# Performance work log

Measured on AMD Instinct MI355X. Metric: run time of the kernel, lower is better.

Reference implementation:

```python
import jax, jax.numpy as jnp
import numpy as np

NPG = 128      # nodes per graph = g(4) * e(32), forced by rearrange + cnn1 channels
G, E32 = 4, 32
ALPHA = 1.0    # GCN2Conv(in_channels, 1) -> alpha = 1
BETA = 1.0     # theta=None -> beta = 1


def _gcn_norm(edge_index, edge_weight, n):
    """PyG gcn_norm: add self-loops (w=1), sym-normalize by degree at dst."""
    src, dst = edge_index[0], edge_index[1]
    loop = jnp.arange(n)
    src = jnp.concatenate([src, loop])
    dst = jnp.concatenate([dst, loop])
    w = jnp.concatenate([edge_weight, jnp.ones((n,), edge_weight.dtype)])
    deg = jax.ops.segment_sum(w, dst, num_segments=n)
    dinv = jnp.where(deg > 0, jax.lax.rsqrt(deg), 0.0)
    norm = dinv[src] * w * dinv[dst]
    return src, dst, norm


def _propagate(x, src, dst, norm, n):
    # gather -> weight -> scatter-add (SpMM)
    return jax.ops.segment_sum(x[src] * norm[:, None], dst, num_segments=n)


def setup_inputs() -> dict:
    key = jax.random.key(0)
    ks = jax.random.split(key, 10)
    N, E, C, H, CH = 65536, 524288, 128, 512, 256
    x = jax.random.normal(ks[0], (N, C), jnp.float32)
    edge_index = jax.random.randint(ks[1], (2, E), 0, N, dtype=jnp.int64)
    edge_attr = jax.random.uniform(ks[2], (E,), jnp.float32)
    w1_gcn2 = jax.random.normal(ks[3], (C, C), jnp.float32) / np.float32(np.sqrt(C))
    w_gcn = jax.random.normal(ks[4], (C, H), jnp.float32) / np.float32(np.sqrt(C))
    b_gcn = jnp.zeros((H,), jnp.float32)
    w_cnn1 = jax.random.normal(ks[5], (H, 4 * H), jnp.float32) / np.float32(np.sqrt(4 * H))
    b_cnn1 = jnp.zeros((H,), jnp.float32)
    w_cnn2 = jax.random.normal(ks[6], (CH, H), jnp.float32) / np.float32(np.sqrt(H))
    b_cnn2 = jnp.zeros((CH,), jnp.float32)
    w_lin = jax.random.normal(ks[7], (32 * CH,), jnp.float32) / np.float32(np.sqrt(32 * CH))
    b_lin = jnp.zeros((), jnp.float32)
    return {"x": x, "edge_attr": edge_attr, "w1_gcn2": w1_gcn2, "w_gcn": w_gcn,
            "b_gcn": b_gcn, "w_cnn1": w_cnn1, "b_cnn1": b_cnn1, "w_cnn2": w_cnn2,
            "b_cnn2": b_cnn2, "w_lin": w_lin, "b_lin": b_lin, "edge_index": edge_index}


def reference(x, edge_attr, w1_gcn2, w_gcn, b_gcn, w_cnn1, b_cnn1, w_cnn2, b_cnn2,
              w_lin, b_lin, edge_index):
    n = x.shape[0]
    bs = n // NPG
    src, dst, norm = _gcn_norm(edge_index, edge_attr, n)

    # GCN2Conv(C, layer=1): h = (1-a)*A_hat x + a*x0; out = (1-b)*h + b*(h @ W1)
    h = _propagate(x, src, dst, norm, n)
    h = h * (1.0 - ALPHA) + ALPHA * x
    h = (1.0 - BETA) * h + BETA * (h @ w1_gcn2)

    # GCNConv(C, H): A_hat (h @ W) + b
    h = _propagate(h @ w_gcn, src, dst, norm, n) + b_gcn
    h = jnp.tanh(h)

    f = h.shape[1]  # hidden_channels
    # '(bs g e) f -> bs (g f) e', e=32, g=4
    h = h.reshape(bs, G, E32, f).transpose(0, 1, 3, 2).reshape(bs, G * f, E32)
    # 1x1 convs == per-position linears over channel dim
    h = jax.nn.relu(jnp.einsum('bce,oc->boe', h, w_cnn1) + b_cnn1[None, :, None])
    h = jax.nn.relu(jnp.einsum('bce,oc->boe', h, w_cnn2) + b_cnn2[None, :, None])
    # dropout p=0.5 is identity in eval mode
    h = h.reshape(bs, -1)
    out = h @ w_lin + b_lin
    return jax.nn.sigmoid(out)
```

## Files before the change

### kernel.cpp

```cpp
#include <hip/hip_runtime.h>
#include <hip/hip_bf16.h>

#define N_NODES 65536
#define N_EDGES 524288

typedef __attribute__((ext_vector_type(8))) short bf16x8;
typedef __attribute__((ext_vector_type(4))) float f32x4;

__device__ __forceinline__ float bf2f(unsigned short u) {
    union { unsigned int i; float f; } v;
    v.i = ((unsigned int)u) << 16;
    return v.f;
}
__device__ __forceinline__ unsigned short f2bf(float f) {
    union { float f; unsigned int i; } v;
    v.f = f;
    unsigned int r = v.i + 0x7fff + ((v.i >> 16) & 1);
    return (unsigned short)(r >> 16);
}

__global__ void init_k(int* __restrict__ cnt, float* __restrict__ logits) {
    int i = blockIdx.x * 256 + threadIdx.x;
    cnt[i] = 0;
    if (i < 512) logits[i] = 0.0f;
}
__global__ void cnt_k(const int* __restrict__ dst, int* __restrict__ cnt) {
    int e = blockIdx.x * 256 + threadIdx.x;
    atomicAdd(&cnt[dst[e]], 1);
}

__global__ __launch_bounds__(256) void scan1_k(const int* __restrict__ cnt,
                                               int* __restrict__ rp,
                                               int* __restrict__ bsum) {
    __shared__ int s[256];
    int t = threadIdx.x, g = blockIdx.x * 256 + t;
    int v = cnt[g];
    s[t] = v;
    __syncthreads();
    for (int d = 1; d < 256; d <<= 1) {
        int u = (t >= d) ? s[t - d] : 0;
        __syncthreads();
        s[t] += u;
        __syncthreads();
    }
    rp[g] = s[t] - v;
    if (t == 255) bsum[blockIdx.x] = s[255];
}
__global__ __launch_bounds__(256) void scan2_k(int* __restrict__ bsum,
                                               int* __restrict__ rp) {
    __shared__ int s[256];
    int t = threadIdx.x;
    int v = bsum[t];
    s[t] = v;
    __syncthreads();
    for (int d = 1; d < 256; d <<= 1) {
        int u = (t >= d) ? s[t - d] : 0;
        __syncthreads();
        s[t] += u;
        __syncthreads();
    }
    bsum[t] = s[t] - v;
    if (t == 255) rp[65536] = s[255];
}
__global__ __launch_bounds__(256) void scan3_k(int* __restrict__ rp,
                                               const int* __restrict__ bsum,
                                               int* __restrict__ cursor) {
    int t = threadIdx.x, g = blockIdx.x * 256 + t;
    int r = rp[g] + bsum[blockIdx.x];
    rp[g] = r;
    cursor[g] = r;
}

__global__ void scatter_k(const int* __restrict__ src, const int* __restrict__ dst,
                          const float* __restrict__ w,
                          int* __restrict__ cursor, uint2* __restrict__ ep) {
    int e = blockIdx.x * 256 + threadIdx.x;
    int pos = atomicAdd(&cursor[dst[e]], 1);
    uint2 p;
    p.x = (unsigned int)src[e];
    p.y = __float_as_uint(w[e]);
    ep[pos] = p;
}

__global__ void rowsum_k(const int* __restrict__ rp, const uint2* __restrict__ ep,
                         float* __restrict__ dinv) {
    int n = blockIdx.x * 256 + threadIdx.x;
    int beg = rp[n], end = rp[n + 1];
    float s = 1.0f;
    for (int i = beg; i < end; ++i) s += __uint_as_float(ep[i].y);
    dinv[n] = rsqrtf(s);
}

__global__ void xscale_k(const float* __restrict__ x, const float* __restrict__ dinv,
                         __hip_bfloat16* __restrict__ xbf) {
    int i = (blockIdx.x * 256 + threadIdx.x) * 4;
    float d = dinv[i >> 7];
    float4 v = *(const float4*)(x + i);
    alignas(8) __hip_bfloat16 tmp[4] = {
        __float2bfloat16(d * v.x), __float2bfloat16(d * v.y),
        __float2bfloat16(d * v.z), __float2bfloat16(d * v.w)};
    *(ushort4*)((unsigned short*)xbf + i) = *(const ushort4*)tmp;
}

__global__ void wprep_k(const float* __restrict__ wc1, __hip_bfloat16* __restrict__ wc1pk,
                        const float* __restrict__ wc2, __hip_bfloat16* __restrict__ wc2bf,
                        const float* __restrict__ w1, const float* __restrict__ wg,
                        __hip_bfloat16* __restrict__ WTpk) {
    int bid = blockIdx.x;
    if (bid < 512) {
        int t = bid * 256 + threadIdx.x;
        int l = t & 63, grp = t >> 6;
        int kt = grp & 63, nb = grp >> 6;
        int n = nb * 16 + (l & 15);
        int k0 = kt * 32 + (l >> 4) * 8;
        const float* src = wc1 + (size_t)n * 2048 + k0;
        alignas(16) __hip_bfloat16 tmp[8];
#pragma unroll
        for (int e = 0; e < 8; ++e) tmp[e] = __float2bfloat16(src[e]);
        *(ushort4*)((unsigned short*)wc1pk + (size_t)t * 8)     = *(const ushort4*)tmp;
        *(ushort4*)((unsigned short*)wc1pk + (size_t)t * 8 + 4) = *(const ushort4*)(tmp + 4);
    } else if (bid < 640) {
        int i = (bid - 512) * 1024 + threadIdx.x * 4;
        float4 v = *(const float4*)(wc2 + i);
        alignas(8) __hip_bfloat16 tmp[4] = {__float2bfloat16(v.x), __float2bfloat16(v.y),
                                            __float2bfloat16(v.z), __float2bfloat16(v.w)};
        *(ushort4*)((unsigned short*)wc2bf + i) = *(const ushort4*)tmp;
    } else {
        int t = (bid - 640) * 256 + threadIdx.x;
        int f = t >> 7, c = t & 127;
        float s = 0.f;
#pragma unroll 8
        for (int m = 0; m < 128; ++m) s += w1[c * 128 + m] * wg[m * 512 + f];
        int pk = ((((f >> 4) * 4 + (c >> 5)) * 64 + ((c >> 3) & 3) * 16 + (f & 15)) * 8) + (c & 7);
        WTpk[pk] = __float2bfloat16(s);
    }
}

__global__ __launch_bounds__(256) void gather_k(const int* __restrict__ rp,
                                                const uint2* __restrict__ ep,
                                                const unsigned short* __restrict__ xbf,
                                                const float* __restrict__ dinv,
                                                __hip_bfloat16* __restrict__ ybf) {
    int n = (blockIdx.x * 256 + threadIdx.x) >> 6;
    int lane = threadIdx.x & 63;
    int beg = rp[n], end = rp[n + 1];
    float accx, accy;
    {
        unsigned int u = *(const unsigned int*)(xbf + (size_t)n * 128 + lane * 2);
        accx = bf2f((unsigned short)(u & 0xffff));
        accy = bf2f((unsigned short)(u >> 16));
    }
    int i = beg;
    for (; i + 8 <= end; i += 8) {
        uint2 p[8];
        unsigned int u[8];
#pragma unroll
        for (int k = 0; k < 8; ++k) p[k] = ep[i + k];
#pragma unroll
        for (int k = 0; k < 8; ++k)
            u[k] = *(const unsigned int*)(xbf + (size_t)p[k].x * 128 + lane * 2);
#pragma unroll
        for (int k = 0; k < 8; ++k) {
            float c = __uint_as_float(p[k].y);
            accx += c * bf2f((unsigned short)(u[k] & 0xffff));
            accy += c * bf2f((unsigned short)(u[k] >> 16));
        }
    }
    for (; i + 4 <= end; i += 4) {
        uint2 p[4];
        unsigned int u[4];
#pragma unroll
        for (int k = 0; k < 4; ++k) p[k] = ep[i + k];
#pragma unroll
        for (int k = 0; k < 4; ++k)
            u[k] = *(const unsigned int*)(xbf + (size_t)p[k].x * 128 + lane * 2);
#pragma unroll
        for (int k = 0; k < 4; ++k) {
            float c = __uint_as_float(p[k].y);
            accx += c * bf2f((unsigned short)(u[k] & 0xffff));
            accy += c * bf2f((unsigned short)(u[k] >> 16));
        }
    }
    for (; i < end; ++i) {
        uint2 p = ep[i];
        unsigned int u = *(const unsigned int*)(xbf + (size_t)p.x * 128 + lane * 2);
        float c = __uint_as_float(p.y);
        accx += c * bf2f((unsigned short)(u & 0xffff));
        accy += c * bf2f((unsigned short)(u >> 16));
    }
    float dn = dinv[n];
    accx *= dn;
    accy *= dn;
    alignas(4) __hip_bfloat16 o[2] = {__float2bfloat16(accx), __float2bfloat16(accy)};
    *(unsigned int*)((unsigned short*)ybf + (size_t)n * 128 + lane * 2) =
        *(const unsigned int*)o;
}

__device__ __forceinline__ void gll16(const void* g, void* l) {
    __builtin_amdgcn_global_load_lds(
        (const __attribute__((address_space(1))) void*)g,
        (__attribute__((address_space(3))) void*)l, 16, 0, 0);
}

__global__ __launch_bounds__(512) void fh2c1_k(
    const __hip_bfloat16* __restrict__ ybf,
    const __hip_bfloat16* __restrict__ WTpk,
    const float* __restrict__ bg,
    const __hip_bfloat16* __restrict__ wc1pk,
    const float* __restrict__ bc1,
    __hip_bfloat16* __restrict__ act1) {
    __shared__ char yt[16384];
    __shared__ char ht[16384];
    const int tid = threadIdx.x;
    const int lane = tid & 63, wid = tid >> 6;
    const int bx = blockIdx.x;
    const int l15 = lane & 15, lhi = lane >> 4;

    const __hip_bfloat16* Bp[4];
#pragma unroll
    for (int j = 0; j < 4; ++j)
        Bp[j] = wc1pk + ((size_t)(wid * 4 + j) * 64) * 512 + lane * 8;

    auto stageY = [&](int buf, int g) {
        int r = wid * 4 + (lane >> 4);
        int node = bx * 128 + g * 32 + r;
        int scol = ((lane & 15) ^ (r & 7)) << 4;
        gll16((const char*)ybf + (size_t)node * 256 + scol,
              yt + buf * 8192 + wid * 1024 + lane * 16);
    };

    f32x4 acc[2][4] = {};

    stageY(0, 0);
    __syncthreads();

    for (int g = 0; g < 4; ++g) {
        if (g > 0) __syncthreads();
        const char* ytc = yt + (g & 1) * 8192;

        for (int h = 0; h < 2; ++h) {
            f32x4 hacc[2][2];
#pragma unroll
            for (int i = 0; i < 2; ++i)
#pragma unroll
                for (int j = 0; j < 2; ++j) hacc[i][j] = (f32x4){0.f, 0.f, 0.f, 0.f};
#pragma unroll
            for (int kt = 0; kt < 4; ++kt) {
                bf16x8 af[2], bfr[2];
#pragma unroll
                for (int i = 0; i < 2; ++i) {
                    int r = i * 16 + l15;
                    int s = (kt * 4 + lhi) ^ (r & 7);
                    af[i] = *(const bf16x8*)(ytc + r * 256 + s * 16);
                }
#pragma unroll
                for (int j = 0; j < 2; ++j) {
                    int nb = h * 16 + wid * 2 + j;
                    bfr[j] = *(const bf16x8*)(WTpk +
                        ((size_t)(nb * 4 + kt) * 64 + lane) * 8);
                }
#pragma unroll
                for (int i = 0; i < 2; ++i)
#pragma unroll
                    for (int j = 0; j < 2; ++j)
                        hacc[i][j] = __builtin_amdgcn_mfma_f32_16x16x32_bf16(
                            bfr[j], af[i], hacc[i][j], 0, 0, 0);
            }
            __syncthreads();
#pragma unroll
            for (int j = 0; j < 2; ++j) {
                int coln = h * 256 + wid * 32 + j * 16 + lhi * 4;
                float4 bgv = *(const float4*)(bg + coln);
                int bytecol = (wid * 32 + j * 16 + lhi * 4) * 2;
                int s = bytecol >> 4;
                int off8 = bytecol & 15;
#pragma unroll
                for (int i = 0; i < 2; ++i) {
                    int row = i * 16 + l15;
                    alignas(8) unsigned short o[4];
#pragma unroll
                    for (int r = 0; r < 4; ++r) {
                        float v = hacc[i][j][r] + ((const float*)&bgv)[r];
                        v = 1.0f - 2.0f / (__expf(2.0f * v) + 1.0f);
                        o[r] = f2bf(v);
                    }
                    *(uint2*)(ht + row * 512 + ((s ^ (row & 7)) << 4) + off8) =
                        *(const uint2*)o;
                }
            }
            __syncthreads();

            if (h == 1 && g < 3) stageY((g + 1) & 1, g + 1);

            const int ktb = g * 16 + h * 8;
            bf16x8 bb[4][4];
#pragma unroll
            for (int d = 0; d < 4; ++d)
#pragma unroll
                for (int j = 0; j < 4; ++j)
                    bb[d][j] = *(const bf16x8*)(Bp[j] + (size_t)(ktb + d) * 512);
#pragma unroll
            for (int kk = 0; kk < 8; ++kk) {
                bf16x8 af[2];
#pragma unroll
                for (int i = 0; i < 2; ++i) {
                    int r = i * 16 + l15;
                    int s = (kk * 4 + lhi) ^ (r & 7);
                    af[i] = *(const bf16x8*)(ht + r * 512 + s * 16);
                }
#pragma unroll
                for (int i = 0; i < 2; ++i)
#pragma unroll
                    for (int j = 0; j < 4; ++j)
                        acc[i][j] = __builtin_amdgcn_mfma_f32_16x16x32_bf16(
                            bb[kk & 3][j], af[i], acc[i][j], 0, 0, 0);
                if (kk + 4 < 8) {
#pragma unroll
                    for (int j = 0; j < 4; ++j)
                        bb[kk & 3][j] =
                            *(const bf16x8*)(Bp[j] + (size_t)(ktb + kk + 4) * 512);
                }
            }
        }
    }

#pragma unroll
    for (int i = 0; i < 2; ++i) {
        int m = bx * 32 + i * 16 + l15;
#pragma unroll
        for (int j = 0; j < 4; ++j) {
            int n = wid * 64 + j * 16 + lhi * 4;
            float4 bv = *(const float4*)(bc1 + n);
            ushort4 o;
#pragma unroll
            for (int r = 0; r < 4; ++r) {
                float v = fmaxf(acc[i][j][r] + ((const float*)&bv)[r], 0.f);
                ((unsigned short*)&o)[r] = f2bf(v);
            }
            *(ushort4*)((unsigned short*)act1 + (size_t)m * 512 + n) = o;
        }
    }
}

template <int ACT, int OUT_MODE, int SWIZ_NTX>
__global__ __launch_bounds__(256) void gemm_mfma_k(
    const __hip_bfloat16* __restrict__ A, const __hip_bfloat16* __restrict__ B,
    const float* __restrict__ bias, void* __restrict__ Cout,
    const float* __restrict__ wlin, int M, int N, int K) {
    __shared__ char lds[65536];

    const int tid = threadIdx.x;
    const int lane = tid & 63, wid = tid >> 6;
    int bx, by;
    if (SWIZ_NTX > 0) {
        int orig = blockIdx.x;
        int per = gridDim.x / (8 * SWIZ_NTX);
        int xcd = orig & 7, k = orig >> 3;
        by = xcd * per + k / SWIZ_NTX;
        bx = k % SWIZ_NTX;
    } else {
        bx = blockIdx.x;
        by = blockIdx.y;
    }
    const int bm = by * 128, bn = bx * 128;
    const int wr = wid >> 1, wc = wid & 1;

    const int srow = wid * 16 + (lane >> 2);
    const int skcol = (((lane & 3) ^ ((lane >> 3) & 3))) * 8;
    const __hip_bfloat16* Abase = A + (size_t)(bm + srow) * K + skcol;
    const __hip_bfloat16* Bbase = B + (size_t)(bn + srow) * K + skcol;
    const int ldso = wid * 1024;

    f32x4 acc[4][4] = {};

    const int lrow = lane & 15;
    const int lkb = (((lane >> 4) ^ ((lane >> 1) & 3)) << 4);
    const int nk = K >> 5;

    auto stage = [&](int buf, int kt) {
        char* la = lds + buf * 16384;
        char* lb = la + 8192;
        gll16(Abase + kt * 32,                  la + ldso);
        gll16(Abase + kt * 32 + (size_t)64 * K, la + 4096 + ldso);
        gll16(Bbase + kt * 32,                  lb + ldso);
        gll16(Bbase + kt * 32 + (size_t)64 * K, lb + 4096 + ldso);
    };

    stage(0, 0);
    stage(1, 1);
    stage(2, 2);

    for (int kt = 0; kt < nk; ++kt) {
        int ahead = nk - 1 - kt;
        if (ahead >= 2)      asm volatile("s_waitcnt vmcnt(8)" ::: "memory");
        else if (ahead == 1) asm volatile("s_waitcnt vmcnt(4)" ::: "memory");
        else                 asm volatile("s_waitcnt vmcnt(0)" ::: "memory");
        __builtin_amdgcn_s_barrier();
        asm volatile("" ::: "memory");
        if (kt + 3 < nk) stage((kt + 3) & 3, kt + 3);

        const char* la = lds + (kt & 3) * 16384;
        const char* lb = la + 8192;
        bf16x8 af[4], bfr[4];
#pragma unroll
        for (int i = 0; i < 4; ++i)
            af[i] = *(const bf16x8*)(la + (wr * 64 + i * 16 + lrow) * 64 + lkb);
#pragma unroll
        for (int j = 0; j < 4; ++j)
            bfr[j] = *(const bf16x8*)(lb + (wc * 64 + j * 16 + lrow) * 64 + lkb);
        __builtin_amdgcn_s_setprio(1);
#pragma unroll
        for (int i = 0; i < 4; ++i)
#pragma unroll
            for (int j = 0; j < 4; ++j)
                acc[i][j] = __builtin_amdgcn_mfma_f32_16x16x32_bf16(
                    bfr[j], af[i], acc[i][j], 0, 0, 0);
        __builtin_amdgcn_s_setprio(0);
        asm volatile("" ::: "memory");
    }

    const int l15 = lane & 15, lhi = lane >> 4;

    if (OUT_MODE == 3) {
        float p0 = 0.f, p1 = 0.f;
#pragma unroll
        for (int i = 0; i < 4; ++i) {
            int e = (i & 1) * 16 + l15;
#pragma unroll
            for (int j = 0; j < 4; ++j) {
                int n = bn + wc * 64 + j * 16 + lhi * 4;
                float4 bv = *(const float4*)(bias + n);
#pragma unroll
                for (int r = 0; r < 4; ++r) {
                    float v = fmaxf(acc[i][j][r] + ((const float*)&bv)[r], 0.f);
                    float wl = wlin[(n + r) * 32 + e];
                    if (i < 2) p0 += v * wl; else p1 += v * wl;
                }
            }
        }
#pragma unroll
        for (int off = 32; off > 0; off >>= 1) {
            p0 += __shfl_down(p0, off, 64);
            p1 += __shfl_down(p1, off, 64);
        }
        if (lane == 0) {
            int g = (bm >> 5) + wr * 2;
            atomicAdd(&((float*)Cout)[g], p0);
            atomicAdd(&((float*)Cout)[g + 1], p1);
        }
        return;
    }

#pragma unroll
    for (int i = 0; i < 4; ++i) {
        int m = bm + wr * 64 + i * 16 + l15;
#pragma unroll
        for (int j = 0; j < 4; ++j) {
            int n = bn + wc * 64 + j * 16 + lhi * 4;
            float4 bv = *(const float4*)(bias + n);
            ushort4 o;
#pragma unroll
            for (int r = 0; r < 4; ++r) {
                float v = acc[i][j][r] + ((const float*)&bv)[r];
                if (ACT == 1) v = fmaxf(v, 0.f);
                ((unsigned short*)&o)[r] = f2bf(v);
            }
            *(ushort4*)((unsigned short*)Cout + (size_t)m * N + n) = o;
        }
    }
}

__global__ void sigmoid_k(const float* __restrict__ logits,
                          const float* __restrict__ blin, float* __restrict__ out) {
    int b = blockIdx.x * 256 + threadIdx.x;
    out[b] = 1.0f / (1.0f + expf(-(logits[b] + blin[0])));
}

extern "C" void kernel_launch(void* const* d_in, const int* in_sizes, int n_in,
                              void* d_out, int out_size, void* d_ws, size_t ws_size,
                              hipStream_t stream) {
    const float* x    = (const float*)d_in[0];
    const float* eattr= (const float*)d_in[1];
    const float* w1   = (const float*)d_in[2];
    const float* wg   = (const float*)d_in[3];
    const float* bg   = (const float*)d_in[4];
    const float* wc1  = (const float*)d_in[5];
    const float* bc1  = (const float*)d_in[6];
    const float* wc2  = (const float*)d_in[7];
    const float* bc2  = (const float*)d_in[8];
    const float* wlin = (const float*)d_in[9];
    const float* blin = (const float*)d_in[10];
    const int*   ei   = (const int*)d_in[11];
    const int* esrc = ei;
    const int* edst = ei + N_EDGES;
    float* out = (float*)d_out;

    char* ws = (char*)d_ws;
    float*          dinv   = (float*)(ws + 0);
    int*            cnt    = (int*)(ws + 262144);
    int*            rp     = (int*)(ws + 524288);
    int*            cursor = (int*)(ws + 786688);
    uint2*          ep     = (uint2*)(ws + 1048832);
    __hip_bfloat16* WTpk   = (__hip_bfloat16*)(ws + 5243136);
    __hip_bfloat16* ybf    = (__hip_bfloat16*)(ws + 5374208);
    __hip_bfloat16* act1   = (__hip_bfloat16*)(ws + 89260288);
    __hip_bfloat16* wc1pk  = (__hip_bfloat16*)(ws + 106037504);
    __hip_bfloat16* wc2bf  = (__hip_bfloat16*)(ws + 108134656);
    __hip_bfloat16* xbf    = (__hip_bfloat16*)(ws + 108396800);
    float*          logits = (float*)(ws + 125174016);
    int*            bsum   = (int*)(ws + 125176064);
    if (ws_size < (size_t)125177088) return;

    init_k<<<N_NODES / 256, 256, 0, stream>>>(cnt, logits);

    cnt_k<<<N_EDGES / 256, 256, 0, stream>>>(edst, cnt);

    scan1_k<<<256, 256, 0, stream>>>(cnt, rp, bsum);
    scan2_k<<<1, 256, 0, stream>>>(bsum, rp);
    scan3_k<<<256, 256, 0, stream>>>(rp, bsum, cursor);

    scatter_k<<<N_EDGES / 256, 256, 0, stream>>>(esrc, edst, eattr, cursor, ep);

    rowsum_k<<<N_NODES / 256, 256, 0, stream>>>(rp, ep, dinv);

    wprep_k<<<896, 256, 0, stream>>>(wc1, wc1pk, wc2, wc2bf, w1, wg, WTpk);
    xscale_k<<<(N_NODES * 128 / 4) / 256, 256, 0, stream>>>(x, dinv, xbf);

    gather_k<<<N_NODES / 4, 256, 0, stream>>>(rp, ep,
                                              (const unsigned short*)xbf, dinv, ybf);

    fh2c1_k<<<512, 512, 0, stream>>>(ybf, WTpk, bg, wc1pk, bc1, act1);

    gemm_mfma_k<1, 3, 0><<<dim3(2, 128), 256, 0, stream>>>(
        act1, wc2bf, bc2, logits, wlin, 16384, 256, 512);

    sigmoid_k<<<2, 256, 0, stream>>>(logits, blin, out);
}
```

Baseline: 195.1 us.

## Fuse cnn2 GEMM, linear head and sigmoid into the cnn1 kernel

The act1 intermediate is no longer written to global memory. The cnn1 output tile is staged into swizzled LDS, and each block then runs the cnn2 GEMM with MFMA against the packed wc2 weights. It applies bias and ReLU, dot-products with w_lin, reduces across waves and writes the sigmoid output for its graph directly. This removes two kernel launches, the act1 round trip and the atomics on logits, at the cost of a longer per-block tail and cnn2 B fragments loaded straight from global memory without LDS staging.

Result: faster. 186.4 us, median of 2 (-4.5%).

```diff
diff --git a/kernel.cpp b/kernel.cpp
--- a/kernel.cpp
+++ b/kernel.cpp
@@ -19,10 +19,8 @@
     return (unsigned short)(r >> 16);
 }
 
-__global__ void init_k(int* __restrict__ cnt, float* __restrict__ logits) {
-    int i = blockIdx.x * 256 + threadIdx.x;
-    cnt[i] = 0;
-    if (i < 512) logits[i] = 0.0f;
+__global__ void init_k(int* __restrict__ cnt) {
+    cnt[blockIdx.x * 256 + threadIdx.x] = 0;
 }
 __global__ void cnt_k(const int* __restrict__ dst, int* __restrict__ cnt) {
     int e = blockIdx.x * 256 + threadIdx.x;
@@ -103,30 +101,28 @@
 }
 
 __global__ void wprep_k(const float* __restrict__ wc1, __hip_bfloat16* __restrict__ wc1pk,
-                        const float* __restrict__ wc2, __hip_bfloat16* __restrict__ wc2bf,
+                        const float* __restrict__ wc2, __hip_bfloat16* __restrict__ wc2pk,
                         const float* __restrict__ w1, const float* __restrict__ wg,
                         __hip_bfloat16* __restrict__ WTpk) {
     int bid = blockIdx.x;
-    if (bid < 512) {
-        int t = bid * 256 + threadIdx.x;
+    if (bid < 576) {
+        const float* W;
+        __hip_bfloat16* outp;
+        int t, K, nkt;
+        if (bid < 512) { W = wc1; outp = wc1pk; t = bid * 256 + threadIdx.x; K = 2048; nkt = 64; }
+        else           { W = wc2; outp = wc2pk; t = (bid - 512) * 256 + threadIdx.x; K = 512; nkt = 16; }
         int l = t & 63, grp = t >> 6;
-        int kt = grp & 63, nb = grp >> 6;
+        int kt = grp % nkt, nb = grp / nkt;
         int n = nb * 16 + (l & 15);
         int k0 = kt * 32 + (l >> 4) * 8;
-        const float* src = wc1 + (size_t)n * 2048 + k0;
+        const float* src = W + (size_t)n * K + k0;
         alignas(16) __hip_bfloat16 tmp[8];
 #pragma unroll
         for (int e = 0; e < 8; ++e) tmp[e] = __float2bfloat16(src[e]);
-        *(ushort4*)((unsigned short*)wc1pk + (size_t)t * 8)     = *(const ushort4*)tmp;
-        *(ushort4*)((unsigned short*)wc1pk + (size_t)t * 8 + 4) = *(const ushort4*)(tmp + 4);
-    } else if (bid < 640) {
-        int i = (bid - 512) * 1024 + threadIdx.x * 4;
-        float4 v = *(const float4*)(wc2 + i);
-        alignas(8) __hip_bfloat16 tmp[4] = {__float2bfloat16(v.x), __float2bfloat16(v.y),
-                                            __float2bfloat16(v.z), __float2bfloat16(v.w)};
-        *(ushort4*)((unsigned short*)wc2bf + i) = *(const ushort4*)tmp;
+        *(ushort4*)((unsigned short*)outp + (size_t)t * 8)     = *(const ushort4*)tmp;
+        *(ushort4*)((unsigned short*)outp + (size_t)t * 8 + 4) = *(const ushort4*)(tmp + 4);
     } else {
-        int t = (bid - 640) * 256 + threadIdx.x;
+        int t = (bid - 576) * 256 + threadIdx.x;
         int f = t >> 7, c = t & 127;
         float s = 0.f;
 #pragma unroll 8
@@ -208,9 +204,15 @@
     const float* __restrict__ bg,
     const __hip_bfloat16* __restrict__ wc1pk,
     const float* __restrict__ bc1,
-    __hip_bfloat16* __restrict__ act1) {
-    __shared__ char yt[16384];
-    __shared__ char ht[16384];
+    const __hip_bfloat16* __restrict__ wc2pk,
+    const float* __restrict__ bc2,
+    const float* __restrict__ wlin,
+    const float* __restrict__ blin,
+    float* __restrict__ out) {
+    __shared__ char lds[32768];
+    __shared__ float red[8];
+    char* yt = lds;
+    char* ht = lds + 16384;
     const int tid = threadIdx.x;
     const int lane = tid & 63, wid = tid >> 6;
     const int bx = blockIdx.x;
@@ -324,156 +326,85 @@
         }
     }
 
-#pragma unroll
-    for (int i = 0; i < 2; ++i) {
-        int m = bx * 32 + i * 16 + l15;
-#pragma unroll
-        for (int j = 0; j < 4; ++j) {
-            int n = wid * 64 + j * 16 + lhi * 4;
-            float4 bv = *(const float4*)(bc1 + n);
-            ushort4 o;
+    __syncthreads();
+    char* at = lds;
+
+#pragma unroll
+    for (int j = 0; j < 4; ++j) {
+        int coln = wid * 64 + j * 16 + lhi * 4;
+        float4 bv = *(const float4*)(bc1 + coln);
+        int bytecol = coln * 2;
+        int s = bytecol >> 4;
+        int off8 = bytecol & 15;
+#pragma unroll
+        for (int i = 0; i < 2; ++i) {
+            int row = i * 16 + l15;
+            alignas(8) unsigned short o[4];
 #pragma unroll
             for (int r = 0; r < 4; ++r) {
                 float v = fmaxf(acc[i][j][r] + ((const float*)&bv)[r], 0.f);
-                ((unsigned short*)&o)[r] = f2bf(v);
+                o[r] = f2bf(v);
             }
-            *(ushort4*)((unsigned short*)act1 + (size_t)m * 512 + n) = o;
-        }
-    }
-}
-
-template <int ACT, int OUT_MODE, int SWIZ_NTX>
-__global__ __launch_bounds__(256) void gemm_mfma_k(
-    const __hip_bfloat16* __restrict__ A, const __hip_bfloat16* __restrict__ B,
-    const float* __restrict__ bias, void* __restrict__ Cout,
-    const float* __restrict__ wlin, int M, int N, int K) {
-    __shared__ char lds[65536];
-
-    const int tid = threadIdx.x;
-    const int lane = tid & 63, wid = tid >> 6;
-    int bx, by;
-    if (SWIZ_NTX > 0) {
-        int orig = blockIdx.x;
-        int per = gridDim.x / (8 * SWIZ_NTX);
-        int xcd = orig & 7, k = orig >> 3;
-        by = xcd * per + k / SWIZ_NTX;
-        bx = k % SWIZ_NTX;
-    } else {
-        bx = blockIdx.x;
-        by = blockIdx.y;
-    }
-    const int bm = by * 128, bn = bx * 128;
-    const int wr = wid >> 1, wc = wid & 1;
-
-    const int srow = wid * 16 + (lane >> 2);
-    const int skcol = (((lane & 3) ^ ((lane >> 3) & 3))) * 8;
-    const __hip_bfloat16* Abase = A + (size_t)(bm + srow) * K + skcol;
-    const __hip_bfloat16* Bbase = B + (size_t)(bn + srow) * K + skcol;
-    const int ldso = wid * 1024;
-
-    f32x4 acc[4][4] = {};
-
-    const int lrow = lane & 15;
-    const int lkb = (((lane >> 4) ^ ((lane >> 1) & 3)) << 4);
-    const int nk = K >> 5;
-
-    auto stage = [&](int buf, int kt) {
-        char* la = lds + buf * 16384;
-        char* lb = la + 8192;
-        gll16(Abase + kt * 32,                  la + ldso);
-        gll16(Abase + kt * 32 + (size_t)64 * K, la + 4096 + ldso);
-        gll16(Bbase + kt * 32,                  lb + ldso);
-        gll16(Bbase + kt * 32 + (size_t)64 * K, lb + 4096 + ldso);
-    };
-
-    stage(0, 0);
-    stage(1, 1);
-    stage(2, 2);
-
-    for (int kt = 0; kt < nk; ++kt) {
-        int ahead = nk - 1 - kt;
-        if (ahead >= 2)      asm volatile("s_waitcnt vmcnt(8)" ::: "memory");
-        else if (ahead == 1) asm volatile("s_waitcnt vmcnt(4)" ::: "memory");
-        else                 asm volatile("s_waitcnt vmcnt(0)" ::: "memory");
-        __builtin_amdgcn_s_barrier();
-        asm volatile("" ::: "memory");
-        if (kt + 3 < nk) stage((kt + 3) & 3, kt + 3);
-
-        const char* la = lds + (kt & 3) * 16384;
-        const char* lb = la + 8192;
-        bf16x8 af[4], bfr[4];
-#pragma unroll
-        for (int i = 0; i < 4; ++i)
-            af[i] = *(const bf16x8*)(la + (wr * 64 + i * 16 + lrow) * 64 + lkb);
-#pragma unroll
-        for (int j = 0; j < 4; ++j)
-            bfr[j] = *(const bf16x8*)(lb + (wc * 64 + j * 16 + lrow) * 64 + lkb);
-        __builtin_amdgcn_s_setprio(1);
-#pragma unroll
-        for (int i = 0; i < 4; ++i)
-#pragma unroll
-            for (int j = 0; j < 4; ++j)
-                acc[i][j] = __builtin_amdgcn_mfma_f32_16x16x32_bf16(
-                    bfr[j], af[i], acc[i][j], 0, 0, 0);
-        __builtin_amdgcn_s_setprio(0);
-        asm volatile("" ::: "memory");
-    }
-
-    const int l15 = lane & 15, lhi = lane >> 4;
-
-    if (OUT_MODE == 3) {
-        float p0 = 0.f, p1 = 0.f;
-#pragma unroll
-        for (int i = 0; i < 4; ++i) {
-            int e = (i & 1) * 16 + l15;
-#pragma unroll
-            for (int j = 0; j < 4; ++j) {
-                int n = bn + wc * 64 + j * 16 + lhi * 4;
-                float4 bv = *(const float4*)(bias + n);
-#pragma unroll
-                for (int r = 0; r < 4; ++r) {
-                    float v = fmaxf(acc[i][j][r] + ((const float*)&bv)[r], 0.f);
-                    float wl = wlin[(n + r) * 32 + e];
-                    if (i < 2) p0 += v * wl; else p1 += v * wl;
-                }
+            *(uint2*)(at + row * 1024 + ((s ^ (row & 7)) << 4) + off8) =
+                *(const uint2*)o;
+        }
+    }
+    __syncthreads();
+
+    const __hip_bfloat16* Cp[2];
+#pragma unroll
+    for (int j = 0; j < 2; ++j)
+        Cp[j] = wc2pk + ((size_t)(wid * 2 + j) * 16) * 512 + lane * 8;
+    f32x4 cacc[2][2];
+#pragma unroll
+    for (int i = 0; i < 2; ++i)
+#pragma unroll
+        for (int j = 0; j < 2; ++j) cacc[i][j] = (f32x4){0.f, 0.f, 0.f, 0.f};
+#pragma unroll
+    for (int kt = 0; kt < 16; ++kt) {
+        bf16x8 af[2], bfr[2];
+#pragma unroll
+        for (int i = 0; i < 2; ++i) {
+            int r = i * 16 + l15;
+            int s = (kt * 4 + lhi) ^ (r & 7);
+            af[i] = *(const bf16x8*)(at + r * 1024 + s * 16);
+        }
+#pragma unroll
+        for (int j = 0; j < 2; ++j)
+            bfr[j] = *(const bf16x8*)(Cp[j] + (size_t)kt * 512);
+#pragma unroll
+        for (int i = 0; i < 2; ++i)
+#pragma unroll
+            for (int j = 0; j < 2; ++j)
+                cacc[i][j] = __builtin_amdgcn_mfma_f32_16x16x32_bf16(
+                    bfr[j], af[i], cacc[i][j], 0, 0, 0);
+    }
+
+    float part = 0.f;
+#pragma unroll
+    for (int i = 0; i < 2; ++i) {
+        int e = i * 16 + l15;
+#pragma unroll
+        for (int j = 0; j < 2; ++j) {
+            int p = wid * 32 + j * 16 + lhi * 4;
+            float4 bv = *(const float4*)(bc2 + p);
+#pragma unroll
+            for (int r = 0; r < 4; ++r) {
+                float v = fmaxf(cacc[i][j][r] + ((const float*)&bv)[r], 0.f);
+                part += v * wlin[(p + r) * 32 + e];
             }
         }
-#pragma unroll
-        for (int off = 32; off > 0; off >>= 1) {
-            p0 += __shfl_down(p0, off, 64);
-            p1 += __shfl_down(p1, off, 64);
-        }
-        if (lane == 0) {
-            int g = (bm >> 5) + wr * 2;
-            atomicAdd(&((float*)Cout)[g], p0);
-            atomicAdd(&((float*)Cout)[g + 1], p1);
-        }
-        return;
-    }
-
-#pragma unroll
-    for (int i = 0; i < 4; ++i) {
-        int m = bm + wr * 64 + i * 16 + l15;
-#pragma unroll
-        for (int j = 0; j < 4; ++j) {
-            int n = bn + wc * 64 + j * 16 + lhi * 4;
-            float4 bv = *(const float4*)(bias + n);
-            ushort4 o;
-#pragma unroll
-            for (int r = 0; r < 4; ++r) {
-                float v = acc[i][j][r] + ((const float*)&bv)[r];
-                if (ACT == 1) v = fmaxf(v, 0.f);
-                ((unsigned short*)&o)[r] = f2bf(v);
-            }
-            *(ushort4*)((unsigned short*)Cout + (size_t)m * N + n) = o;
-        }
-    }
-}
-
-__global__ void sigmoid_k(const float* __restrict__ logits,
-                          const float* __restrict__ blin, float* __restrict__ out) {
-    int b = blockIdx.x * 256 + threadIdx.x;
-    out[b] = 1.0f / (1.0f + expf(-(logits[b] + blin[0])));
+    }
+#pragma unroll
+    for (int off = 32; off > 0; off >>= 1) part += __shfl_down(part, off, 64);
+    if (lane == 0) red[wid] = part;
+    __syncthreads();
+    if (tid == 0) {
+        float tot = blin[0];
+#pragma unroll
+        for (int w = 0; w < 8; ++w) tot += red[w];
+        out[bx] = 1.0f / (1.0f + __expf(-tot));
+    }
 }
 
 extern "C" void kernel_launch(void* const* d_in, const int* in_sizes, int n_in,
@@ -503,15 +434,13 @@
     uint2*          ep     = (uint2*)(ws + 1048832);
     __hip_bfloat16* WTpk   = (__hip_bfloat16*)(ws + 5243136);
     __hip_bfloat16* ybf    = (__hip_bfloat16*)(ws + 5374208);
-    __hip_bfloat16* act1   = (__hip_bfloat16*)(ws + 89260288);
-    __hip_bfloat16* wc1pk  = (__hip_bfloat16*)(ws + 106037504);
-    __hip_bfloat16* wc2bf  = (__hip_bfloat16*)(ws + 108134656);
-    __hip_bfloat16* xbf    = (__hip_bfloat16*)(ws + 108396800);
-    float*          logits = (float*)(ws + 125174016);
-    int*            bsum   = (int*)(ws + 125176064);
-    if (ws_size < (size_t)125177088) return;
-
-    init_k<<<N_NODES / 256, 256, 0, stream>>>(cnt, logits);
+    __hip_bfloat16* wc1pk  = (__hip_bfloat16*)(ws + 22151424);
+    __hip_bfloat16* wc2pk  = (__hip_bfloat16*)(ws + 24248576);
+    __hip_bfloat16* xbf    = (__hip_bfloat16*)(ws + 24510720);
+    int*            bsum   = (int*)(ws + 41287936);
+    if (ws_size < (size_t)41288960) return;
+
+    init_k<<<N_NODES / 256, 256, 0, stream>>>(cnt);
 
     cnt_k<<<N_EDGES / 256, 256, 0, stream>>>(edst, cnt);
 
@@ -523,16 +452,12 @@
 
     rowsum_k<<<N_NODES / 256, 256, 0, stream>>>(rp, ep, dinv);
 
-    wprep_k<<<896, 256, 0, stream>>>(wc1, wc1pk, wc2, wc2bf, w1, wg, WTpk);
+    wprep_k<<<832, 256, 0, stream>>>(wc1, wc1pk, wc2, wc2pk, w1, wg, WTpk);
     xscale_k<<<(N_NODES * 128 / 4) / 256, 256, 0, stream>>>(x, dinv, xbf);
 
     gather_k<<<N_NODES / 4, 256, 0, stream>>>(rp, ep,
                                               (const unsigned short*)xbf, dinv, ybf);
 
-    fh2c1_k<<<512, 512, 0, stream>>>(ybf, WTpk, bg, wc1pk, bc1, act1);
-
-    gemm_mfma_k<1, 3, 0><<<dim3(2, 128), 256, 0, stream>>>(
-        act1, wc2bf, bc2, logits, wlin, 16384, 256, 512);
-
-    sigmoid_k<<<2, 256, 0, stream>>>(logits, blin, out);
-}
+    fh2c1_k<<<512, 512, 0, stream>>>(ybf, WTpk, bg, wc1pk, bc1,
+                                     wc2pk, bc2, wlin, blin, out);
+}
```
